# Kernel optimization log

Hardware: AMD Instinct MI355X
Metric: run time of the kernel (lower is better)

## Reference

```python
import jax, jax.numpy as jnp
import numpy as np

B, T, D, H = 2, 4096, 768, 12
DH = D // H


def setup_inputs() -> dict:
    key = jax.random.key(0)
    ks = jax.random.split(key, 4)
    x = jax.random.normal(ks[0], (B, T, D), dtype=jnp.float32)
    Wqkv = jax.random.normal(ks[1], (D, 3 * D), dtype=jnp.float32) * (D ** -0.5)
    bqkv = jnp.zeros((3 * D,), dtype=jnp.float32)
    Wproj = jax.random.normal(ks[2], (D, D), dtype=jnp.float32) * (D ** -0.5)
    bproj = jnp.zeros((D,), dtype=jnp.float32)
    return {"x": x, "Wqkv": Wqkv, "bqkv": bqkv, "Wproj": Wproj, "bproj": bproj}


def reference(x, Wqkv, bqkv, Wproj, bproj):
    b, t, c = x.shape
    qkv = x @ Wqkv + bqkv                      # [B,T,3D]
    qkv = qkv.reshape(b, t, H, 3 * DH)
    q, k, v = jnp.split(qkv, 3, axis=-1)       # each [B,T,H,DH]
    q = q.transpose(0, 2, 1, 3)                # [B,H,T,DH]
    k = k.transpose(0, 2, 1, 3)
    v = v.transpose(0, 2, 1, 3)
    att = jnp.einsum('bhqd,bhkd->bhqk', q, k) / (DH ** 0.5)  # [B,H,T,T]
    mask = jnp.tril(jnp.ones((t, t), dtype=bool))
    att = jnp.where(mask, att, jnp.float32(-1e9))
    att = jax.nn.softmax(att, axis=-1)
    out = jnp.einsum('bhqk,bhkd->bhqd', att, v)  # [B,H,T,DH]
    out = out.transpose(0, 2, 1, 3).reshape(b, t, c)
    return out @ Wproj + bproj
```

## Files before the change

kernel.cpp:

```cpp
#include <hip/hip_runtime.h>

typedef unsigned short u16;
typedef unsigned int u32;
typedef __bf16 bf16x8 __attribute__((ext_vector_type(8)));
typedef float f32x4 __attribute__((ext_vector_type(4)));
typedef float f32x16 __attribute__((ext_vector_type(16)));
typedef u16 u16x4 __attribute__((ext_vector_type(4)));
typedef u32 u32x2 __attribute__((ext_vector_type(2)));
typedef u32 u32x4 __attribute__((ext_vector_type(4)));

#define QSCALE 0.18033688011112042f
#define MFIX 12.0f

static __device__ __forceinline__ u16 f2bf(float f) {
  __bf16 h = (__bf16)f;
  return __builtin_bit_cast(u16, h);
}

static __device__ __forceinline__ u32 pk2(float a, float b) {
  return (u32)f2bf(a) | ((u32)f2bf(b) << 16);
}

static __device__ __forceinline__ void gl_lds16(const void* g, void* l) {
  __builtin_amdgcn_global_load_lds(
      (const __attribute__((address_space(1))) unsigned int*)g,
      (__attribute__((address_space(3))) unsigned int*)l, 16, 0, 0);
}

static __device__ __forceinline__ void wait_vmcnt8() {
  asm volatile("s_waitcnt vmcnt(8)" ::: "memory");
  __builtin_amdgcn_sched_barrier(0);
}
static __device__ __forceinline__ void wait_vmcnt4() {
  asm volatile("s_waitcnt vmcnt(4)" ::: "memory");
  __builtin_amdgcn_sched_barrier(0);
}
static __device__ __forceinline__ void wait_vmcnt0() {
  asm volatile("s_waitcnt vmcnt(0)" ::: "memory");
  __builtin_amdgcn_sched_barrier(0);
}
static __device__ __forceinline__ void barrier_mem() {
  asm volatile("s_barrier" ::: "memory");
  __builtin_amdgcn_sched_barrier(0);
}

static __device__ __forceinline__ f32x16 zero16() {
  f32x16 z;
#pragma unroll
  for (int i = 0; i < 16; ++i) z[i] = 0.f;
  return z;
}

__global__ void k_cvt(const float* __restrict__ in, u16* __restrict__ out, int n4) {
  int i = blockIdx.x * 256 + threadIdx.x;
  if (i < n4) {
    f32x4 f = ((const f32x4*)in)[i];
    u16x4 u = { f2bf(f[0]), f2bf(f[1]), f2bf(f[2]), f2bf(f[3]) };
    ((u16x4*)out)[i] = u;
  }
}

__global__ void k_transpose_cvt(const float* __restrict__ in, u16* __restrict__ out,
                                int R, int C) {
  __shared__ float tile[32][33];
  const int c0 = blockIdx.x * 32, r0 = blockIdx.y * 32;
  const int tx = threadIdx.x, ty = threadIdx.y;
#pragma unroll
  for (int i = 0; i < 4; ++i)
    tile[ty + i * 8][tx] = in[(size_t)(r0 + ty + i * 8) * C + c0 + tx];
  __syncthreads();
#pragma unroll
  for (int i = 0; i < 4; ++i)
    out[(size_t)(c0 + ty + i * 8) * R + r0 + tx] = f2bf(tile[tx][ty + i * 8]);
}

static __device__ __forceinline__ void gemm_core(const u16* __restrict__ Ag,
                                                 const u16* __restrict__ Btg,
                                                 int K, int m0, int n0,
                                                 u16* As, u16* Bs,
                                                 f32x4 acc[4][4]) {
  const int tid = threadIdx.x;
  const int lane = tid & 63;
  const int wid = tid >> 6;
  const int wm = wid >> 1, wn = wid & 1;
  const int l16 = lane & 15, lg = lane >> 4;

  for (int kt = 0; kt < K; kt += 64) {
    __syncthreads();
#pragma unroll
    for (int i = 0; i < 4; ++i) {
      int chunk = i * 256 + tid;
      int row = chunk >> 3;
      int lcb = ((chunk & 7) << 4) ^ ((row & 7) << 4);
      gl_lds16(Ag + (size_t)(m0 + row) * K + kt + (lcb >> 1),
               As + ((i * 256 + wid * 64) << 3));
    }
#pragma unroll
    for (int i = 0; i < 4; ++i) {
      int chunk = i * 256 + tid;
      int row = chunk >> 3;
      int lcb = ((chunk & 7) << 4) ^ ((row & 7) << 4);
      gl_lds16(Btg + (size_t)(n0 + row) * K + kt + (lcb >> 1),
               Bs + ((i * 256 + wid * 64) << 3));
    }
    __syncthreads();

#pragma unroll
    for (int ks = 0; ks < 2; ++ks) {
      bf16x8 af[4], bfr[4];
#pragma unroll
      for (int mi = 0; mi < 4; ++mi) {
        int row = wm * 64 + mi * 16 + l16;
        int off = row * 128 + ((ks * 64 + (lg << 4)) ^ ((row & 7) << 4));
        af[mi] = *(const bf16x8*)((const char*)As + off);
      }
#pragma unroll
      for (int ni = 0; ni < 4; ++ni) {
        int row = wn * 64 + ni * 16 + l16;
        int off = row * 128 + ((ks * 64 + (lg << 4)) ^ ((row & 7) << 4));
        bfr[ni] = *(const bf16x8*)((const char*)Bs + off);
      }
#pragma unroll
      for (int mi = 0; mi < 4; ++mi)
#pragma unroll
        for (int ni = 0; ni < 4; ++ni)
          acc[mi][ni] = __builtin_amdgcn_mfma_f32_16x16x32_bf16(
              af[mi], bfr[ni], acc[mi][ni], 0, 0, 0);
    }
  }
}

__global__ __launch_bounds__(256) void k_gemm_qkv(
    const u16* __restrict__ A, const u16* __restrict__ Bt,
    const float* __restrict__ bias, u16* __restrict__ Q, u16* __restrict__ Kb,
    u16* __restrict__ Vt) {
  __shared__ __align__(16) u16 As[128 * 64];
  __shared__ __align__(16) u16 Bs[128 * 64];
  const int m0 = blockIdx.y * 128, n0 = blockIdx.x * 128;
  const f32x4 fz = {0.f, 0.f, 0.f, 0.f};
  f32x4 acc[4][4];
#pragma unroll
  for (int mi = 0; mi < 4; ++mi)
#pragma unroll
    for (int ni = 0; ni < 4; ++ni) acc[mi][ni] = fz;

  gemm_core(A, Bt, 768, m0, n0, As, Bs, acc);

  const int tid = threadIdx.x, lane = tid & 63, wid = tid >> 6;
  const int wm = wid >> 1, wn = wid & 1, l16 = lane & 15, lg = lane >> 4;
#pragma unroll
  for (int mi = 0; mi < 4; ++mi)
#pragma unroll
    for (int ni = 0; ni < 4; ++ni) {
      int n = n0 + wn * 64 + ni * 16 + l16;
      float bi = bias[n];
      int h = n / 192;
      int rr = n - h * 192;
      int m0w = m0 + wm * 64 + mi * 16 + lg * 4;
      int bb = m0w >> 12, t0 = m0w & 4095;
      size_t base = ((size_t)(bb * 12 + h) * 4096 + t0) * 64;
      if (rr < 64) {
#pragma unroll
        for (int r = 0; r < 4; ++r)
          Q[base + (size_t)r * 64 + rr] = f2bf((acc[mi][ni][r] + bi) * QSCALE);
      } else if (rr < 128) {
#pragma unroll
        for (int r = 0; r < 4; ++r)
          Kb[base + (size_t)r * 64 + rr - 64] = f2bf(acc[mi][ni][r] + bi);
      } else {
        u16x4 vv;
#pragma unroll
        for (int r = 0; r < 4; ++r) vv[r] = f2bf(acc[mi][ni][r] + bi);
        *(u16x4*)(Vt + ((size_t)(bb * 12 + h) * 64 + (rr - 128)) * 4096 + t0) = vv;
      }
    }
}

__global__ __launch_bounds__(256) void k_gemm_proj(
    const u16* __restrict__ A, const u16* __restrict__ Bt,
    const float* __restrict__ bias, float* __restrict__ out) {
  __shared__ __align__(16) u16 As[128 * 64];
  __shared__ __align__(16) u16 Bs[128 * 64];
  const int m0 = blockIdx.y * 128, n0 = blockIdx.x * 128;
  const f32x4 fz = {0.f, 0.f, 0.f, 0.f};
  f32x4 acc[4][4];
#pragma unroll
  for (int mi = 0; mi < 4; ++mi)
#pragma unroll
    for (int ni = 0; ni < 4; ++ni) acc[mi][ni] = fz;

  gemm_core(A, Bt, 768, m0, n0, As, Bs, acc);

  const int tid = threadIdx.x, lane = tid & 63, wid = tid >> 6;
  const int wm = wid >> 1, wn = wid & 1, l16 = lane & 15, lg = lane >> 4;
#pragma unroll
  for (int mi = 0; mi < 4; ++mi)
#pragma unroll
    for (int ni = 0; ni < 4; ++ni) {
      int n = n0 + wn * 64 + ni * 16 + l16;
      float bi = bias[n];
#pragma unroll
      for (int r = 0; r < 4; ++r) {
        int m = m0 + wm * 64 + mi * 16 + lg * 4 + r;
        out[(size_t)m * 768 + n] = acc[mi][ni][r] + bi;
      }
    }
}

__global__ __launch_bounds__(128) void k_attn(const u16* __restrict__ Qg,
                                              const u16* __restrict__ Kg,
                                              const u16* __restrict__ Vtg,
                                              u16* __restrict__ Og) {
  __shared__ __align__(16) u16 Ks[2][64 * 64];
  __shared__ __align__(16) u16 Vs[64 * 64];
  const int bid = blockIdx.x;
  const int xcd = bid & 7;
  const int u = bid >> 3;
  const int s = u & 31;
  const int rnd = u >> 5;
  const int bh = xcd * 3 + (rnd >> 1);
  const int jX = (rnd & 1) ? s : (63 - s);
  const int tid = threadIdx.x;
  const int lane = tid & 63;
  const int wid = tid >> 6;
  const int l32 = lane & 31;
  const int hi = lane >> 5;
  const int rxor = (l32 & 7) << 4;
  const size_t qk_base = (size_t)bh * (4096 * 64);
  const size_t vt_base = (size_t)bh * (64 * 4096);
  const int b = bh / 12, h = bh - b * 12;

  const int q0w = jX * 64 + wid * 32;
  const int qrow = q0w + l32;
  const int nkt = jX + 1;

  int coK[4], coVa[4], coVb[4];
#pragma unroll
  for (int st = 0; st < 4; ++st) coK[st] = (st * 32 + hi * 16) ^ rxor;
#pragma unroll
  for (int ks = 0; ks < 4; ++ks) {
    coVa[ks] = (ks * 32 + hi * 8) ^ rxor;
    coVb[ks] = (ks * 32 + 16 + hi * 8) ^ rxor;
  }
  const int rb0 = l32 * 128, rb1 = (32 + l32) * 128;

  const int trow = tid >> 3;
  const int tcol = ((((tid & 7) << 4) ^ ((trow & 7) << 4)) >> 1);
  const int tdst = tid << 3;
  const u16* kp0 = Kg + qk_base + (size_t)trow * 64 + tcol;
  const u16* kp1 = kp0 + (size_t)16 * 64;
  const u16* kp2 = kp0 + (size_t)32 * 64;
  const u16* kp3 = kp0 + (size_t)48 * 64;
  const u16* vq0 = Vtg + vt_base + (size_t)trow * 4096 + tcol;
  const u16* vq1 = vq0 + (size_t)16 * 4096;
  const u16* vq2 = vq0 + (size_t)32 * 4096;
  const u16* vq3 = vq0 + (size_t)48 * 4096;

  auto stageK = [&](u16* Kd) {
    gl_lds16(kp0, Kd + tdst);
    gl_lds16(kp1, Kd + 1024 + tdst);
    gl_lds16(kp2, Kd + 2048 + tdst);
    gl_lds16(kp3, Kd + 3072 + tdst);
    kp0 += 4096; kp1 += 4096; kp2 += 4096; kp3 += 4096;
  };
  auto stageV = [&]() {
    gl_lds16(vq0, Vs + tdst);
    gl_lds16(vq1, Vs + 1024 + tdst);
    gl_lds16(vq2, Vs + 2048 + tdst);
    gl_lds16(vq3, Vs + 3072 + tdst);
    vq0 += 64; vq1 += 64; vq2 += 64; vq3 += 64;
  };

  bf16x8 qb[4];
#pragma unroll
  for (int st = 0; st < 4; ++st)
    qb[st] = *(const bf16x8*)(Qg + qk_base + (size_t)qrow * 64 + st * 16 + hi * 8);

  f32x16 o0 = zero16(), o1 = zero16();
  float lrun = 0.f;

  stageK(Ks[0]);

  for (int kt = 0; kt < nkt; ++kt) {
    const bool more = (kt + 1 < nkt);
    stageV();
    if (more) stageK(Ks[(kt + 1) & 1]);
    if (more) wait_vmcnt8(); else wait_vmcnt4();
    barrier_mem();

    const bool diag = (kt == nkt - 1);
    const bool halfskip = diag && (wid == 0);
    const char* Kbp = (const char*)Ks[kt & 1];
    const char* Vb = (const char*)Vs;

    f32x16 s0 = zero16(), s1 = zero16();
    __builtin_amdgcn_s_setprio(1);
#pragma unroll
    for (int st = 0; st < 4; ++st) {
      bf16x8 ka0 = *(const bf16x8*)(Kbp + rb0 + coK[st]);
      s0 = __builtin_amdgcn_mfma_f32_32x32x16_bf16(ka0, qb[st], s0, 0, 0, 0);
    }
    if (!halfskip) {
#pragma unroll
      for (int st = 0; st < 4; ++st) {
        bf16x8 ka1 = *(const bf16x8*)(Kbp + rb1 + coK[st]);
        s1 = __builtin_amdgcn_mfma_f32_32x32x16_bf16(ka1, qb[st], s1, 0, 0, 0);
      }
    }
    __builtin_amdgcn_s_setprio(0);

    if (diag) {
      const int kbase = kt * 64 + 4 * hi;
#pragma unroll
      for (int r = 0; r < 16; ++r) {
        int kpv = kbase + (r & 3) + 8 * (r >> 2);
        s0[r] = (kpv > qrow) ? -3.0e38f : s0[r];
        if (!halfskip) s1[r] = (kpv + 32 > qrow) ? -3.0e38f : s1[r];
      }
    }

#pragma unroll
    for (int r = 0; r < 16; ++r) {
      s0[r] = __builtin_amdgcn_exp2f(s0[r] - MFIX);
      if (!halfskip) s1[r] = __builtin_amdgcn_exp2f(s1[r] - MFIX);
    }

    float a8[8];
#pragma unroll
    for (int r = 0; r < 8; ++r) {
      float v = s0[r] + s0[r + 8];
      if (!halfskip) v += s1[r] + s1[r + 8];
      a8[r] = v;
    }
    lrun += ((a8[0] + a8[1]) + (a8[2] + a8[3])) +
            ((a8[4] + a8[5]) + (a8[6] + a8[7]));

    if (more) wait_vmcnt4(); else wait_vmcnt0();
    barrier_mem();

    __builtin_amdgcn_s_setprio(1);
#pragma unroll
    for (int ks = 0; ks < 4; ++ks) {
      if (ks >= 2 && halfskip) continue;
      const f32x16& P = (ks >= 2) ? s1 : s0;
      const int base = (ks & 1) * 8;
      u32x4 w = { pk2(P[base + 0], P[base + 1]), pk2(P[base + 2], P[base + 3]),
                  pk2(P[base + 4], P[base + 5]), pk2(P[base + 6], P[base + 7]) };
      bf16x8 pbk = __builtin_bit_cast(bf16x8, w);
      u32x2 q0 = *(const u32x2*)(Vb + rb0 + coVa[ks]);
      u32x2 q1 = *(const u32x2*)(Vb + rb0 + coVb[ks]);
      u32x4 av = {q0[0], q0[1], q1[0], q1[1]};
      bf16x8 va0 = __builtin_bit_cast(bf16x8, av);
      o0 = __builtin_amdgcn_mfma_f32_32x32x16_bf16(va0, pbk, o0, 0, 0, 0);
      u32x2 p0 = *(const u32x2*)(Vb + rb1 + coVa[ks]);
      u32x2 p1 = *(const u32x2*)(Vb + rb1 + coVb[ks]);
      u32x4 bv = {p0[0], p0[1], p1[0], p1[1]};
      bf16x8 va1 = __builtin_bit_cast(bf16x8, bv);
      o1 = __builtin_amdgcn_mfma_f32_32x32x16_bf16(va1, pbk, o1, 0, 0, 0);
    }
    __builtin_amdgcn_s_setprio(0);

    barrier_mem();
  }

  float lt = lrun + __shfl_xor(lrun, 32, 64);
  float inv = 1.0f / lt;
  u16* orow = Og + ((size_t)b * 4096 + qrow) * 768 + h * 64;
#pragma unroll
  for (int gg = 0; gg < 4; ++gg) {
    u16x4 v0, v1;
#pragma unroll
    for (int i = 0; i < 4; ++i) {
      v0[i] = f2bf(o0[4 * gg + i] * inv);
      v1[i] = f2bf(o1[4 * gg + i] * inv);
    }
    *(u16x4*)(orow + 8 * gg + 4 * hi) = v0;
    *(u16x4*)(orow + 32 + 8 * gg + 4 * hi) = v1;
  }
}

extern "C" void kernel_launch(void* const* d_in, const int* in_sizes, int n_in,
                              void* d_out, int out_size, void* d_ws, size_t ws_size,
                              hipStream_t stream) {
  const float* x = (const float*)d_in[0];
  const float* Wqkv = (const float*)d_in[1];
  const float* bqkv = (const float*)d_in[2];
  const float* Wproj = (const float*)d_in[3];
  const float* bproj = (const float*)d_in[4];
  float* out = (float*)d_out;

  char* ws = (char*)d_ws;
  u16* Xbf = (u16*)(ws + 0);
  u16* WqkvT = (u16*)(ws + 12582912);
  u16* WprojT = (u16*)(ws + 16121856);
  u16* Q = (u16*)(ws + 17301504);
  u16* K = (u16*)(ws + 29884416);
  u16* Vt = (u16*)(ws + 42467328);
  u16* O = (u16*)(ws + 55050240);

  k_cvt<<<6144, 256, 0, stream>>>(x, Xbf, 1572864);
  k_transpose_cvt<<<dim3(72, 24), dim3(32, 8), 0, stream>>>(Wqkv, WqkvT, 768, 2304);
  k_transpose_cvt<<<dim3(24, 24), dim3(32, 8), 0, stream>>>(Wproj, WprojT, 768, 768);
  k_gemm_qkv<<<dim3(18, 64), 256, 0, stream>>>(Xbf, WqkvT, bqkv, Q, K, Vt);
  k_attn<<<1536, 128, 0, stream>>>(Q, K, Vt, O);
  k_gemm_proj<<<dim3(6, 64), 256, 0, stream>>>(O, WprojT, bproj, out);
}
```

Measured before the change: 199.3 us.

## Double-buffer V with K in attention and stage QKV epilogue through LDS

```diff
diff --git a/kernel.cpp b/kernel.cpp
--- a/kernel.cpp
+++ b/kernel.cpp
@@ -6,6 +6,7 @@
 typedef float f32x4 __attribute__((ext_vector_type(4)));
 typedef float f32x16 __attribute__((ext_vector_type(16)));
 typedef u16 u16x4 __attribute__((ext_vector_type(4)));
+typedef u16 u16x8 __attribute__((ext_vector_type(8)));
 typedef u32 u32x2 __attribute__((ext_vector_type(2)));
 typedef u32 u32x4 __attribute__((ext_vector_type(4)));
 
@@ -27,14 +28,6 @@
       (__attribute__((address_space(3))) unsigned int*)l, 16, 0, 0);
 }
 
-static __device__ __forceinline__ void wait_vmcnt8() {
-  asm volatile("s_waitcnt vmcnt(8)" ::: "memory");
-  __builtin_amdgcn_sched_barrier(0);
-}
-static __device__ __forceinline__ void wait_vmcnt4() {
-  asm volatile("s_waitcnt vmcnt(4)" ::: "memory");
-  __builtin_amdgcn_sched_barrier(0);
-}
 static __device__ __forceinline__ void wait_vmcnt0() {
   asm volatile("s_waitcnt vmcnt(0)" ::: "memory");
   __builtin_amdgcn_sched_barrier(0);
@@ -134,8 +127,9 @@
     const u16* __restrict__ A, const u16* __restrict__ Bt,
     const float* __restrict__ bias, u16* __restrict__ Q, u16* __restrict__ Kb,
     u16* __restrict__ Vt) {
-  __shared__ __align__(16) u16 As[128 * 64];
-  __shared__ __align__(16) u16 Bs[128 * 64];
+  __shared__ __align__(16) u16 SH[128 * 128];
+  u16* As = SH;
+  u16* Bs = SH + 128 * 64;
   const int m0 = blockIdx.y * 128, n0 = blockIdx.x * 128;
   const f32x4 fz = {0.f, 0.f, 0.f, 0.f};
   f32x4 acc[4][4];
@@ -145,6 +139,7 @@
     for (int ni = 0; ni < 4; ++ni) acc[mi][ni] = fz;
 
   gemm_core(A, Bt, 768, m0, n0, As, Bs, acc);
+  __syncthreads();
 
   const int tid = threadIdx.x, lane = tid & 63, wid = tid >> 6;
   const int wm = wid >> 1, wn = wid & 1, l16 = lane & 15, lg = lane >> 4;
@@ -152,28 +147,44 @@
   for (int mi = 0; mi < 4; ++mi)
 #pragma unroll
     for (int ni = 0; ni < 4; ++ni) {
-      int n = n0 + wn * 64 + ni * 16 + l16;
+      int nl = wn * 64 + ni * 16 + l16;
+      int n = n0 + nl;
       float bi = bias[n];
       int h = n / 192;
       int rr = n - h * 192;
-      int m0w = m0 + wm * 64 + mi * 16 + lg * 4;
-      int bb = m0w >> 12, t0 = m0w & 4095;
-      size_t base = ((size_t)(bb * 12 + h) * 4096 + t0) * 64;
-      if (rr < 64) {
-#pragma unroll
-        for (int r = 0; r < 4; ++r)
-          Q[base + (size_t)r * 64 + rr] = f2bf((acc[mi][ni][r] + bi) * QSCALE);
-      } else if (rr < 128) {
-#pragma unroll
-        for (int r = 0; r < 4; ++r)
-          Kb[base + (size_t)r * 64 + rr - 64] = f2bf(acc[mi][ni][r] + bi);
-      } else {
+      int ml = wm * 64 + mi * 16 + lg * 4;
+      if (rr >= 128) {
+        int m0w = m0 + ml;
+        int bb = m0w >> 12, t0 = m0w & 4095;
         u16x4 vv;
 #pragma unroll
         for (int r = 0; r < 4; ++r) vv[r] = f2bf(acc[mi][ni][r] + bi);
         *(u16x4*)(Vt + ((size_t)(bb * 12 + h) * 64 + (rr - 128)) * 4096 + t0) = vv;
-      }
-    }
+      } else {
+        float sc = (rr < 64) ? QSCALE : 1.0f;
+#pragma unroll
+        for (int r = 0; r < 4; ++r)
+          SH[(ml + r) * 128 + nl] = f2bf((acc[mi][ni][r] + bi) * sc);
+      }
+    }
+  __syncthreads();
+
+  const int bb2 = m0 >> 12, tb = m0 & 4095;
+#pragma unroll
+  for (int i = 0; i < 8; ++i) {
+    int id = i * 256 + tid;
+    int row = id >> 4;
+    int c = id & 15;
+    int n = n0 + c * 8;
+    int h = n / 192;
+    int rr = n - h * 192;
+    if (rr < 128) {
+      u16x8 v = *(const u16x8*)(SH + row * 128 + c * 8);
+      size_t base = ((size_t)(bb2 * 12 + h) * 4096 + tb + row) * 64;
+      u16* dst = (rr < 64) ? (Q + base + rr) : (Kb + base + rr - 64);
+      *(u16x8*)dst = v;
+    }
+  }
 }
 
 __global__ __launch_bounds__(256) void k_gemm_proj(
@@ -212,7 +223,7 @@
                                               const u16* __restrict__ Vtg,
                                               u16* __restrict__ Og) {
   __shared__ __align__(16) u16 Ks[2][64 * 64];
-  __shared__ __align__(16) u16 Vs[64 * 64];
+  __shared__ __align__(16) u16 Vs[2][64 * 64];
   const int bid = blockIdx.x;
   const int xcd = bid & 7;
   const int u = bid >> 3;
@@ -256,18 +267,16 @@
   const u16* vq2 = vq0 + (size_t)32 * 4096;
   const u16* vq3 = vq0 + (size_t)48 * 4096;
 
-  auto stageK = [&](u16* Kd) {
-    gl_lds16(kp0, Kd + tdst);
-    gl_lds16(kp1, Kd + 1024 + tdst);
-    gl_lds16(kp2, Kd + 2048 + tdst);
-    gl_lds16(kp3, Kd + 3072 + tdst);
+  auto stage = [&](int buf) {
+    gl_lds16(kp0, Ks[buf] + tdst);
+    gl_lds16(kp1, Ks[buf] + 1024 + tdst);
+    gl_lds16(kp2, Ks[buf] + 2048 + tdst);
+    gl_lds16(kp3, Ks[buf] + 3072 + tdst);
+    gl_lds16(vq0, Vs[buf] + tdst);
+    gl_lds16(vq1, Vs[buf] + 1024 + tdst);
+    gl_lds16(vq2, Vs[buf] + 2048 + tdst);
+    gl_lds16(vq3, Vs[buf] + 3072 + tdst);
     kp0 += 4096; kp1 += 4096; kp2 += 4096; kp3 += 4096;
-  };
-  auto stageV = [&]() {
-    gl_lds16(vq0, Vs + tdst);
-    gl_lds16(vq1, Vs + 1024 + tdst);
-    gl_lds16(vq2, Vs + 2048 + tdst);
-    gl_lds16(vq3, Vs + 3072 + tdst);
     vq0 += 64; vq1 += 64; vq2 += 64; vq3 += 64;
   };
 
@@ -279,19 +288,17 @@
   f32x16 o0 = zero16(), o1 = zero16();
   float lrun = 0.f;
 
-  stageK(Ks[0]);
+  stage(0);
 
   for (int kt = 0; kt < nkt; ++kt) {
-    const bool more = (kt + 1 < nkt);
-    stageV();
-    if (more) stageK(Ks[(kt + 1) & 1]);
-    if (more) wait_vmcnt8(); else wait_vmcnt4();
+    wait_vmcnt0();
     barrier_mem();
+    if (kt + 1 < nkt) stage((kt + 1) & 1);
 
     const bool diag = (kt == nkt - 1);
     const bool halfskip = diag && (wid == 0);
     const char* Kbp = (const char*)Ks[kt & 1];
-    const char* Vb = (const char*)Vs;
+    const char* Vb = (const char*)Vs[kt & 1];
 
     f32x16 s0 = zero16(), s1 = zero16();
     __builtin_amdgcn_s_setprio(1);
@@ -334,9 +341,6 @@
     }
     lrun += ((a8[0] + a8[1]) + (a8[2] + a8[3])) +
             ((a8[4] + a8[5]) + (a8[6] + a8[7]));
-
-    if (more) wait_vmcnt4(); else wait_vmcnt0();
-    barrier_mem();
 
     __builtin_amdgcn_s_setprio(1);
 #pragma unroll
@@ -359,8 +363,6 @@
       o1 = __builtin_amdgcn_mfma_f32_32x32x16_bf16(va1, pbk, o1, 0, 0, 0);
     }
     __builtin_amdgcn_s_setprio(0);
-
-    barrier_mem();
   }
 
   float lt = lrun + __shfl_xor(lrun, 32, 64);
```

Result: slower. 228.8 us (+14.8%).

## Stage Q/K epilogue through LDS for 16-byte coalesced stores; drop sched barriers

Applied to the files above, without the earlier changes.

```diff
diff --git a/kernel.cpp b/kernel.cpp
--- a/kernel.cpp
+++ b/kernel.cpp
@@ -6,6 +6,7 @@
 typedef float f32x4 __attribute__((ext_vector_type(4)));
 typedef float f32x16 __attribute__((ext_vector_type(16)));
 typedef u16 u16x4 __attribute__((ext_vector_type(4)));
+typedef u16 u16x8 __attribute__((ext_vector_type(8)));
 typedef u32 u32x2 __attribute__((ext_vector_type(2)));
 typedef u32 u32x4 __attribute__((ext_vector_type(4)));
 
@@ -29,19 +30,15 @@
 
 static __device__ __forceinline__ void wait_vmcnt8() {
   asm volatile("s_waitcnt vmcnt(8)" ::: "memory");
-  __builtin_amdgcn_sched_barrier(0);
 }
 static __device__ __forceinline__ void wait_vmcnt4() {
   asm volatile("s_waitcnt vmcnt(4)" ::: "memory");
-  __builtin_amdgcn_sched_barrier(0);
 }
 static __device__ __forceinline__ void wait_vmcnt0() {
   asm volatile("s_waitcnt vmcnt(0)" ::: "memory");
-  __builtin_amdgcn_sched_barrier(0);
 }
 static __device__ __forceinline__ void barrier_mem() {
   asm volatile("s_barrier" ::: "memory");
-  __builtin_amdgcn_sched_barrier(0);
 }
 
 static __device__ __forceinline__ f32x16 zero16() {
@@ -134,8 +131,9 @@
     const u16* __restrict__ A, const u16* __restrict__ Bt,
     const float* __restrict__ bias, u16* __restrict__ Q, u16* __restrict__ Kb,
     u16* __restrict__ Vt) {
-  __shared__ __align__(16) u16 As[128 * 64];
-  __shared__ __align__(16) u16 Bs[128 * 64];
+  __shared__ __align__(16) u16 SH[128 * 128];
+  u16* As = SH;
+  u16* Bs = SH + 128 * 64;
   const int m0 = blockIdx.y * 128, n0 = blockIdx.x * 128;
   const f32x4 fz = {0.f, 0.f, 0.f, 0.f};
   f32x4 acc[4][4];
@@ -145,6 +143,7 @@
     for (int ni = 0; ni < 4; ++ni) acc[mi][ni] = fz;
 
   gemm_core(A, Bt, 768, m0, n0, As, Bs, acc);
+  __syncthreads();
 
   const int tid = threadIdx.x, lane = tid & 63, wid = tid >> 6;
   const int wm = wid >> 1, wn = wid & 1, l16 = lane & 15, lg = lane >> 4;
@@ -152,28 +151,44 @@
   for (int mi = 0; mi < 4; ++mi)
 #pragma unroll
     for (int ni = 0; ni < 4; ++ni) {
-      int n = n0 + wn * 64 + ni * 16 + l16;
+      int nl = wn * 64 + ni * 16 + l16;
+      int n = n0 + nl;
       float bi = bias[n];
       int h = n / 192;
       int rr = n - h * 192;
-      int m0w = m0 + wm * 64 + mi * 16 + lg * 4;
-      int bb = m0w >> 12, t0 = m0w & 4095;
-      size_t base = ((size_t)(bb * 12 + h) * 4096 + t0) * 64;
-      if (rr < 64) {
-#pragma unroll
-        for (int r = 0; r < 4; ++r)
-          Q[base + (size_t)r * 64 + rr] = f2bf((acc[mi][ni][r] + bi) * QSCALE);
-      } else if (rr < 128) {
-#pragma unroll
-        for (int r = 0; r < 4; ++r)
-          Kb[base + (size_t)r * 64 + rr - 64] = f2bf(acc[mi][ni][r] + bi);
-      } else {
+      int ml = wm * 64 + mi * 16 + lg * 4;
+      if (rr >= 128) {
+        int m0w = m0 + ml;
+        int bb = m0w >> 12, t0 = m0w & 4095;
         u16x4 vv;
 #pragma unroll
         for (int r = 0; r < 4; ++r) vv[r] = f2bf(acc[mi][ni][r] + bi);
         *(u16x4*)(Vt + ((size_t)(bb * 12 + h) * 64 + (rr - 128)) * 4096 + t0) = vv;
-      }
-    }
+      } else {
+        float sc = (rr < 64) ? QSCALE : 1.0f;
+#pragma unroll
+        for (int r = 0; r < 4; ++r)
+          SH[(ml + r) * 128 + nl] = f2bf((acc[mi][ni][r] + bi) * sc);
+      }
+    }
+  __syncthreads();
+
+  const int bb2 = m0 >> 12, tb = m0 & 4095;
+#pragma unroll
+  for (int i = 0; i < 8; ++i) {
+    int id = i * 256 + tid;
+    int row = id >> 4;
+    int c = id & 15;
+    int n = n0 + c * 8;
+    int h = n / 192;
+    int rr = n - h * 192;
+    if (rr < 128) {
+      u16x8 v = *(const u16x8*)(SH + row * 128 + c * 8);
+      size_t base = ((size_t)(bb2 * 12 + h) * 4096 + tb + row) * 64;
+      u16* dst = (rr < 64) ? (Q + base + rr) : (Kb + base + rr - 64);
+      *(u16x8*)dst = v;
+    }
+  }
 }
 
 __global__ __launch_bounds__(256) void k_gemm_proj(
```

Result: no change. 197.7 us (-0.8%).
